# Kernel tuning notes

Measured on AMD Instinct MI355X. Metric: run time of the kernel, lower is better.

## Reference

```python
import jax, jax.numpy as jnp
import numpy as np

B, C, H, W = 2, 256, 360, 360
N1 = N2 = 1024


def setup_inputs() -> dict:
    key = jax.random.key(0)
    ks = jax.random.split(key, 12)
    s = 0.02
    feature = jax.random.normal(ks[0], (B, C, H, W), dtype=jnp.float32)
    # midx rows: [batch_idx, h, w]; frame 0 centers and frame 1 centers
    idx1 = jnp.stack([
        jnp.zeros((N1,), dtype=jnp.int32),
        jax.random.randint(ks[1], (N1,), 0, H, dtype=jnp.int32),
        jax.random.randint(ks[2], (N1,), 0, W, dtype=jnp.int32),
    ])
    idx2 = jnp.stack([
        jnp.ones((N2,), dtype=jnp.int32),
        jax.random.randint(ks[3], (N2,), 0, H, dtype=jnp.int32),
        jax.random.randint(ks[4], (N2,), 0, W, dtype=jnp.int32),
    ])
    w1 = jax.random.normal(ks[5], (256, 256), dtype=jnp.float32) * s
    b1 = jnp.zeros((256,), dtype=jnp.float32)
    w2 = jax.random.normal(ks[6], (256, 128), dtype=jnp.float32) * s
    b2 = jnp.zeros((128,), dtype=jnp.float32)
    w3 = jax.random.normal(ks[7], (128, 32), dtype=jnp.float32) * s
    b3 = jnp.zeros((32,), dtype=jnp.float32)
    w4 = jax.random.normal(ks[8], (32, 1), dtype=jnp.float32) * s
    b4 = jnp.zeros((1,), dtype=jnp.float32)
    return {"feature": feature, "idx1": idx1, "idx2": idx2,
            "w1": w1, "b1": b1, "w2": w2, "b2": b2,
            "w3": w3, "b3": b3, "w4": w4, "b4": b4}


def reference(feature, idx1, idx2, w1, b1, w2, b2, w3, b3, w4, b4):
    # feature: [B,C,H,W] -> [B,H,W,C] (torch .permute(0,2,3,1))
    feat = jnp.transpose(feature, (0, 2, 3, 1))

    def project(midx):
        # irregular gather of per-center features: [N, C]
        x = feat[midx[0], midx[1], midx[2]]
        h = jax.nn.relu(x @ w1 + b1)          # [N, 256]
        return jax.nn.relu(h @ w2 + b2)       # [N, 128]

    f1 = project(idx1)                        # [N1, D]
    f2 = project(idx2)                        # [N2, D]
    # laplacian_dists: broadcast outer difference [N1, N2, D]
    diff = f1[:, None, :] - f2[None, :, :]
    # out_layer = linear_last(D, 32, 1): Linear -> ReLU -> Linear
    h = jax.nn.relu(jnp.einsum('mnd,dk->mnk', diff, w3) + b3)
    out = jnp.einsum('mnk,ko->mno', h, w4) + b4
    return out[..., 0]                        # [N1, N2] similarity
```

## Files before the change

kernel.cpp:

```cpp
#include <hip/hip_runtime.h>

#define NPTS 1024
#define NC 256
#define NH 360
#define NW 360
#define NHW (NH * NW)
#define NCHW (NC * NHW)
#define PPB 8

__global__ __launch_bounds__(256) void project_kernel(
    const float* __restrict__ feature,
    const int* __restrict__ idx1,
    const int* __restrict__ idx2,
    const float* __restrict__ w1, const float* __restrict__ b1,
    const float* __restrict__ w2, const float* __restrict__ b2,
    const float* __restrict__ w3, const float* __restrict__ b3,
    float* __restrict__ pq)
{
    __shared__ float Xs[PPB * 256];
    __shared__ float H1s[PPB * 256];
    __shared__ float F2s[PPB * 128];

    const int tid = threadIdx.x;
    const int base = blockIdx.x * PPB;

    #pragma unroll
    for (int p = 0; p < PPB; ++p) {
        int point = base + p;
        int col = (point < NPTS) ? point : (point - NPTS);
        const int* idx = (point < NPTS) ? idx1 : idx2;
        int bb = idx[col];
        int hh = idx[NPTS + col];
        int ww = idx[2 * NPTS + col];
        Xs[p * 256 + tid] =
            feature[(size_t)bb * NCHW + (size_t)tid * NHW + hh * NW + ww];
    }
    __syncthreads();

    {
        float acc[PPB];
        #pragma unroll
        for (int p = 0; p < PPB; ++p) acc[p] = 0.f;
        #pragma unroll 4
        for (int c = 0; c < 256; ++c) {
            float wv = w1[c * 256 + tid];
            #pragma unroll
            for (int p = 0; p < PPB; ++p)
                acc[p] = fmaf(Xs[p * 256 + c], wv, acc[p]);
        }
        float bv = b1[tid];
        #pragma unroll
        for (int p = 0; p < PPB; ++p)
            H1s[p * 256 + tid] = fmaxf(acc[p] + bv, 0.f);
    }
    __syncthreads();

    {
        const int j = tid & 127;
        const int half = tid >> 7;
        float acc[4];
        #pragma unroll
        for (int q = 0; q < 4; ++q) acc[q] = 0.f;
        #pragma unroll 4
        for (int c = 0; c < 256; ++c) {
            float wv = w2[c * 128 + j];
            #pragma unroll
            for (int q = 0; q < 4; ++q)
                acc[q] = fmaf(H1s[(half * 4 + q) * 256 + c], wv, acc[q]);
        }
        float bv = b2[j];
        #pragma unroll
        for (int q = 0; q < 4; ++q)
            F2s[(half * 4 + q) * 128 + j] = fmaxf(acc[q] + bv, 0.f);
    }
    __syncthreads();

    {
        const int j = tid & 31;
        const int g = tid >> 5;
        float acc = 0.f;
        #pragma unroll 4
        for (int c = 0; c < 128; ++c)
            acc = fmaf(F2s[g * 128 + c], w3[c * 32 + j], acc);
        int point = base + g;
        float val = (point < NPTS) ? acc : (b3[j] - acc);
        pq[(size_t)point * 32 + j] = val;
    }
}

__global__ __launch_bounds__(256) void pair_kernel(
    const float* __restrict__ pq,
    const float* __restrict__ w4,
    const float* __restrict__ b4,
    float* __restrict__ out)
{
    __shared__ float P1s[16 * 32];
    __shared__ float w4s[32];

    const int tid = threadIdx.x;
    const int n = blockIdx.x * 256 + tid;
    const int m0 = blockIdx.y * 16;

    float q[32];
    const float* q2 = pq + (size_t)(NPTS + n) * 32;
    #pragma unroll
    for (int k = 0; k < 32; ++k) q[k] = q2[k];

    for (int i = tid; i < 16 * 32; i += 256) P1s[i] = pq[(size_t)m0 * 32 + i];
    if (tid < 32) w4s[tid] = w4[tid];
    __syncthreads();

    const float b4v = b4[0];
    #pragma unroll 2
    for (int mm = 0; mm < 16; ++mm) {
        float acc = b4v;
        #pragma unroll
        for (int k = 0; k < 32; ++k) {
            float t = P1s[mm * 32 + k] + q[k];
            acc = fmaf(w4s[k], fmaxf(t, 0.f), acc);
        }
        out[(size_t)(m0 + mm) * 1024 + n] = acc;
    }
}

extern "C" void kernel_launch(void* const* d_in, const int* in_sizes, int n_in,
                              void* d_out, int out_size, void* d_ws, size_t ws_size,
                              hipStream_t stream) {
    const float* feature = (const float*)d_in[0];
    const int*   idx1    = (const int*)d_in[1];
    const int*   idx2    = (const int*)d_in[2];
    const float* w1      = (const float*)d_in[3];
    const float* b1      = (const float*)d_in[4];
    const float* w2      = (const float*)d_in[5];
    const float* b2      = (const float*)d_in[6];
    const float* w3      = (const float*)d_in[7];
    const float* b3      = (const float*)d_in[8];
    const float* w4      = (const float*)d_in[9];
    const float* b4      = (const float*)d_in[10];
    float* out = (float*)d_out;

    float* pq = (float*)d_ws;

    project_kernel<<<2048 / PPB, 256, 0, stream>>>(
        feature, idx1, idx2, w1, b1, w2, b2, w3, b3, pq);

    pair_kernel<<<dim3(1024 / 256, 1024 / 16), 256, 0, stream>>>(
        pq, w4, b4, out);
}
```

Measured before the change: 399.2 us.

## Split gather into separate kernel, widen MLP blocks, shrink pair tiles

Moves the feature gather into its own kernel with one block per point, so many more independent scattered loads are in flight across the GPU. The MLP kernel now uses 512 threads per block, with each thread computing fewer outputs per layer, which gives more parallelism on only 256 blocks. The pair kernel processes 8 rows per block instead of 16, doubling its grid. The cost is an extra kernel launch and a round trip of the gathered features through workspace memory.

```diff
diff --git a/kernel.cpp b/kernel.cpp
--- a/kernel.cpp
+++ b/kernel.cpp
@@ -8,10 +8,25 @@
 #define NCHW (NC * NHW)
 #define PPB 8
 
-__global__ __launch_bounds__(256) void project_kernel(
+__global__ __launch_bounds__(256) void gather_kernel(
     const float* __restrict__ feature,
     const int* __restrict__ idx1,
     const int* __restrict__ idx2,
+    float* __restrict__ X)
+{
+    const int point = blockIdx.x;
+    const int col = point & (NPTS - 1);
+    const int* idx = (point < NPTS) ? idx1 : idx2;
+    const int bb = idx[col];
+    const int hh = idx[NPTS + col];
+    const int ww = idx[2 * NPTS + col];
+    const size_t base = (size_t)bb * NCHW + (size_t)hh * NW + ww;
+    const int c = threadIdx.x;
+    X[(size_t)point * NC + c] = feature[base + (size_t)c * NHW];
+}
+
+__global__ __launch_bounds__(512) void mlp_kernel(
+    const float* __restrict__ X,
     const float* __restrict__ w1, const float* __restrict__ b1,
     const float* __restrict__ w2, const float* __restrict__ b2,
     const float* __restrict__ w3, const float* __restrict__ b3,
@@ -24,58 +39,51 @@
     const int tid = threadIdx.x;
     const int base = blockIdx.x * PPB;
 
-    #pragma unroll
-    for (int p = 0; p < PPB; ++p) {
-        int point = base + p;
-        int col = (point < NPTS) ? point : (point - NPTS);
-        const int* idx = (point < NPTS) ? idx1 : idx2;
-        int bb = idx[col];
-        int hh = idx[NPTS + col];
-        int ww = idx[2 * NPTS + col];
-        Xs[p * 256 + tid] =
-            feature[(size_t)bb * NCHW + (size_t)tid * NHW + hh * NW + ww];
+    {
+        const float* src = X + (size_t)base * 256;
+        #pragma unroll
+        for (int i = 0; i < PPB * 256; i += 512)
+            Xs[i + tid] = src[i + tid];
     }
     __syncthreads();
 
     {
-        float acc[PPB];
-        #pragma unroll
-        for (int p = 0; p < PPB; ++p) acc[p] = 0.f;
+        const int j = tid & 255;
+        const int half = tid >> 8;
+        float acc[4] = {0.f, 0.f, 0.f, 0.f};
         #pragma unroll 4
         for (int c = 0; c < 256; ++c) {
-            float wv = w1[c * 256 + tid];
+            float wv = w1[c * 256 + j];
             #pragma unroll
-            for (int p = 0; p < PPB; ++p)
-                acc[p] = fmaf(Xs[p * 256 + c], wv, acc[p]);
+            for (int q = 0; q < 4; ++q)
+                acc[q] = fmaf(Xs[(half * 4 + q) * 256 + c], wv, acc[q]);
         }
-        float bv = b1[tid];
+        float bv = b1[j];
         #pragma unroll
-        for (int p = 0; p < PPB; ++p)
-            H1s[p * 256 + tid] = fmaxf(acc[p] + bv, 0.f);
+        for (int q = 0; q < 4; ++q)
+            H1s[(half * 4 + q) * 256 + j] = fmaxf(acc[q] + bv, 0.f);
     }
     __syncthreads();
 
     {
         const int j = tid & 127;
-        const int half = tid >> 7;
-        float acc[4];
-        #pragma unroll
-        for (int q = 0; q < 4; ++q) acc[q] = 0.f;
+        const int quad = tid >> 7;
+        float acc[2] = {0.f, 0.f};
         #pragma unroll 4
         for (int c = 0; c < 256; ++c) {
             float wv = w2[c * 128 + j];
             #pragma unroll
-            for (int q = 0; q < 4; ++q)
-                acc[q] = fmaf(H1s[(half * 4 + q) * 256 + c], wv, acc[q]);
+            for (int q = 0; q < 2; ++q)
+                acc[q] = fmaf(H1s[(quad * 2 + q) * 256 + c], wv, acc[q]);
         }
         float bv = b2[j];
         #pragma unroll
-        for (int q = 0; q < 4; ++q)
-            F2s[(half * 4 + q) * 128 + j] = fmaxf(acc[q] + bv, 0.f);
+        for (int q = 0; q < 2; ++q)
+            F2s[(quad * 2 + q) * 128 + j] = fmaxf(acc[q] + bv, 0.f);
     }
     __syncthreads();
 
-    {
+    if (tid < 256) {
         const int j = tid & 31;
         const int g = tid >> 5;
         float acc = 0.f;
@@ -94,25 +102,25 @@
     const float* __restrict__ b4,
     float* __restrict__ out)
 {
-    __shared__ float P1s[16 * 32];
+    __shared__ float P1s[8 * 32];
     __shared__ float w4s[32];
 
     const int tid = threadIdx.x;
     const int n = blockIdx.x * 256 + tid;
-    const int m0 = blockIdx.y * 16;
+    const int m0 = blockIdx.y * 8;
 
     float q[32];
     const float* q2 = pq + (size_t)(NPTS + n) * 32;
     #pragma unroll
     for (int k = 0; k < 32; ++k) q[k] = q2[k];
 
-    for (int i = tid; i < 16 * 32; i += 256) P1s[i] = pq[(size_t)m0 * 32 + i];
+    if (tid < 8 * 32) P1s[tid] = pq[(size_t)m0 * 32 + tid];
     if (tid < 32) w4s[tid] = w4[tid];
     __syncthreads();
 
     const float b4v = b4[0];
-    #pragma unroll 2
-    for (int mm = 0; mm < 16; ++mm) {
+    #pragma unroll
+    for (int mm = 0; mm < 8; ++mm) {
         float acc = b4v;
         #pragma unroll
         for (int k = 0; k < 32; ++k) {
@@ -139,11 +147,13 @@
     const float* b4      = (const float*)d_in[10];
     float* out = (float*)d_out;
 
-    float* pq = (float*)d_ws;
+    float* X  = (float*)d_ws;
+    float* pq = (float*)d_ws + 2048 * 256;
 
-    project_kernel<<<2048 / PPB, 256, 0, stream>>>(
-        feature, idx1, idx2, w1, b1, w2, b2, w3, b3, pq);
+    gather_kernel<<<2048, 256, 0, stream>>>(feature, idx1, idx2, X);
 
-    pair_kernel<<<dim3(1024 / 256, 1024 / 16), 256, 0, stream>>>(
-        pq, w4, b4, out);
+    mlp_kernel<<<2048 / PPB, 512, 0, stream>>>(
+        X, w1, b1, w2, b2, w3, b3, pq);
+
+    pair_kernel<<<dim3(4, 128), 256, 0, stream>>>(pq, w4, b4, out);
 }
```

After: 402.3 us. About the same (+0.8%).
